# Optimization experiments

Measured on AMD Instinct MI355X. Metric: run time of the kernel, lower is better.

## Reference

```python
import jax, jax.numpy as jnp
import numpy as np

NUM_HEADS = 16
HEAD_DIM = 64
WINDOW = 128        # local attention radius |i-j| <= WINDOW
GLOBAL_STRIDE = 64  # tokens at multiples of GLOBAL_STRIDE attend/are attended globally
NEG_INF = -1e9


def sparse_mask(seq_len):
    # bool [S, S]: local band plus global rows/cols (Longformer-style pattern)
    i = jnp.arange(seq_len)
    local = jnp.abs(i[:, None] - i[None, :]) <= WINDOW
    is_global = (i % GLOBAL_STRIDE) == 0
    return local | is_global[:, None] | is_global[None, :]


def setup_inputs() -> dict:
    key = jax.random.key(0)
    k1, k2, k3 = jax.random.split(key, 3)
    B, S, H = 1, 2048, 1024
    x = jax.random.normal(k1, (B, S, H), dtype=jnp.float32)
    Wqkv = jax.random.normal(k2, (3 * H, H), dtype=jnp.float32) * (1.0 / np.sqrt(H))
    Wout = jax.random.normal(k3, (H, H), dtype=jnp.float32) * (1.0 / np.sqrt(H))
    return {"x": x, "Wqkv": Wqkv, "Wout": Wout}


def reference(x, Wqkv, Wout):
    B, S, H = x.shape
    hd = HEAD_DIM
    scale = 1.0 / np.sqrt(hd)

    qkv = x @ Wqkv.T                       # [B, S, 3H] (torch Linear: x @ W^T)
    q, k, v = jnp.split(qkv, 3, axis=-1)
    # [B, nH, S, hd]
    q = q.reshape(B, S, NUM_HEADS, hd).transpose(0, 2, 1, 3)
    k = k.reshape(B, S, NUM_HEADS, hd).transpose(0, 2, 1, 3)
    v = v.reshape(B, S, NUM_HEADS, hd).transpose(0, 2, 1, 3)

    mask = sparse_mask(S)                  # [S, S] bool, broadcasts over (B, nH)
    scores = jnp.einsum('bhqd,bhkd->bhqk', q, k) * scale
    scores = jnp.where(mask, scores, NEG_INF)
    attn = jax.nn.softmax(scores, axis=-1)  # every row has valid keys -> no NaN
    out = jnp.einsum('bhqk,bhkd->bhqd', attn, v)
    out = out.transpose(0, 2, 1, 3).reshape(B, S, H)
    return out @ Wout.T
```

## Files before the change

kernel.cpp:

```cpp
#include <hip/hip_runtime.h>
#include <hip/hip_bf16.h>
#include <math.h>

#define SEQ   2048
#define HID   1024
#define NH    16
#define HD    64
#define WIN   128
#define GSTR  64
#define NSPL  8

typedef __attribute__((ext_vector_type(8))) short short8;
typedef __attribute__((ext_vector_type(4))) float f32x4;
typedef unsigned short ushort_t;

__device__ inline unsigned short bf16b(float f) {
    union { float f; unsigned int u; } v; v.f = f;
    return (unsigned short)((v.u + 0x7FFFu + ((v.u >> 16) & 1u)) >> 16);
}

#define GLOAD_LDS16(gp, lp)                                                    \
    __builtin_amdgcn_global_load_lds(                                          \
        (const __attribute__((address_space(1))) unsigned int*)(gp),           \
        (__attribute__((address_space(3))) unsigned int*)(lp), 16, 0, 0)

__global__ __launch_bounds__(256) void cvt_bf16(const float4* __restrict__ x,
                                                const float4* __restrict__ wq,
                                                const float4* __restrict__ wo,
                                                ushort4* __restrict__ x16,
                                                ushort4* __restrict__ wq16,
                                                ushort4* __restrict__ wo16) {
    for (int idx = blockIdx.x * 256 + threadIdx.x; idx < 1572864;
         idx += gridDim.x * 256) {
        const float4* src; ushort4* dst; int off;
        if (idx < 524288)       { src = x;  dst = x16;  off = idx; }
        else if (idx < 1310720) { src = wq; dst = wq16; off = idx - 524288; }
        else                    { src = wo; dst = wo16; off = idx - 1310720; }
        float4 v = src[off];
        ushort4 o;
        o.x = bf16b(v.x); o.y = bf16b(v.y); o.z = bf16b(v.z); o.w = bf16b(v.w);
        dst[off] = o;
    }
}

template <int BM, int BN, typename OT>
__global__ __launch_bounds__(256) void gemm_bt16(const unsigned short* __restrict__ A,
                                                 const unsigned short* __restrict__ B,
                                                 OT* __restrict__ C,
                                                 int M, int N, int K) {
    constexpr int MI = BM / 32;
    constexpr int NJ = BN / 32;
    __shared__ unsigned short As[2][BM * 32];
    __shared__ unsigned short Bs[2][BN * 32];

    const int tid  = threadIdx.x;
    const int wave = tid >> 6;
    const int lane = tid & 63;
    const int quad = lane >> 4;
    const int l15  = lane & 15;
    const int bm = blockIdx.y * BM;
    const int bn = blockIdx.x * BN;
    const int wm = (wave & 1) * (BM / 2);
    const int wn = (wave >> 1) * (BN / 2);
    const int srow = lane >> 2;
    const int scol = (lane & 3) * 8;

    f32x4 acc[MI][NJ];
    #pragma unroll
    for (int i = 0; i < MI; ++i)
        #pragma unroll
        for (int j = 0; j < NJ; ++j)
            acc[i][j] = (f32x4){0.f, 0.f, 0.f, 0.f};

    for (int k0 = 0; k0 < K; k0 += 64) {
        #pragma unroll
        for (int hh = 0; hh < 2; ++hh) {
            #pragma unroll
            for (int t = 0; t < BM / 64; ++t) {
                const int row = wave * (BM / 4) + t * 16 + srow;
                GLOAD_LDS16(A + (size_t)(bm + row) * K + k0 + hh * 32 + scol,
                            &As[hh][(size_t)row * 32 + scol]);
            }
            #pragma unroll
            for (int t = 0; t < BN / 64; ++t) {
                const int row = wave * (BN / 4) + t * 16 + srow;
                GLOAD_LDS16(B + (size_t)(bn + row) * K + k0 + hh * 32 + scol,
                            &Bs[hh][(size_t)row * 32 + scol]);
            }
        }
        __syncthreads();

        #pragma unroll
        for (int hh = 0; hh < 2; ++hh) {
            short8 a[MI], b[NJ];
            #pragma unroll
            for (int im = 0; im < MI; ++im)
                a[im] = *(const short8*)&As[hh][(wm + im * 16 + l15) * 32 + quad * 8];
            #pragma unroll
            for (int jn = 0; jn < NJ; ++jn)
                b[jn] = *(const short8*)&Bs[hh][(wn + jn * 16 + l15) * 32 + quad * 8];

            #pragma unroll
            for (int im = 0; im < MI; ++im)
                #pragma unroll
                for (int jn = 0; jn < NJ; ++jn)
                    acc[im][jn] = __builtin_amdgcn_mfma_f32_16x16x32_bf16(
                        b[jn], a[im], acc[im][jn], 0, 0, 0);
        }
        __syncthreads();
    }

    #pragma unroll
    for (int im = 0; im < MI; ++im)
        #pragma unroll
        for (int jn = 0; jn < NJ; ++jn) {
            const int r = bm + wm + im * 16 + l15;
            const int c = bn + wn + jn * 16 + quad * 4;
            if constexpr (sizeof(OT) == 2) {
                ushort4 o;
                o.x = bf16b(acc[im][jn][0]);
                o.y = bf16b(acc[im][jn][1]);
                o.z = bf16b(acc[im][jn][2]);
                o.w = bf16b(acc[im][jn][3]);
                *(ushort4*)&C[(size_t)r * N + c] = o;
            } else {
                *(f32x4*)&C[(size_t)r * N + c] = acc[im][jn];
            }
        }
}

__global__ __launch_bounds__(256) void attn_fused(const unsigned short* __restrict__ qkv16,
                                                  unsigned short* __restrict__ aout16,
                                                  float* __restrict__ pO,
                                                  float* __restrict__ pM,
                                                  float* __restrict__ pL) {
    __shared__ __align__(16) unsigned char smem[38912];
    const int tid = threadIdx.x;
    const int h = blockIdx.y;
    const int w    = tid >> 6;
    const int lane = tid & 63;
    const int quad = lane >> 4;
    const int l15  = lane & 15;

    if (blockIdx.x < 32) {
        ushort_t* Qs = (ushort_t*)smem;
        ushort_t* Ks = (ushort_t*)(smem + 9216);
        ushort_t* Vt = (ushort_t*)(smem + 18432);
        ushort_t* Ps = (ushort_t*)(smem + 27648);

        const int bq = blockIdx.x;
        const int q0 = bq * 64;
        const int qi = q0 + w * 16 + l15;

        for (int f = tid; f < 512; f += 256) {
            int row = f >> 3, c8 = f & 7;
            *(uint4*)&Qs[row * 72 + c8 * 8] =
                *(const uint4*)&qkv16[(size_t)(q0 + row) * (3 * HID) + h * HD + c8 * 8];
        }

        float mq = -1.0e30f, lq = 0.f;
        f32x4 Oacc[4];
        #pragma unroll
        for (int jt = 0; jt < 4; ++jt) Oacc[jt] = (f32x4){0.f, 0.f, 0.f, 0.f};

        const int t0 = max(bq - 2, 0);
        const int t1 = min(bq + 2, SEQ / 64 - 1);

        uint4 pk[2];
        uint2 pva[2], pvb[2];

        auto prefetch = [&](int tt2, bool g2) {
            const int nf = g2 ? 256 : 512;
            #pragma unroll
            for (int u = 0; u < 2; ++u) {
                const int f = tid + u * 256;
                if (f < nf) {
                    const int row = f >> 3, c8 = f & 7;
                    const size_t gb = (size_t)(g2 ? (row << 6) : (tt2 * 64 + row))
                                          * (3 * HID) + HID + h * HD + c8 * 8;
                    pk[u] = *(const uint4*)&qkv16[gb];
                    const int kp = f >> 4, dc = f & 15;
                    const int k0i = 2 * kp, k1i = 2 * kp + 1;
                    const size_t b0 = (size_t)(g2 ? (k0i << 6) : (tt2 * 64 + k0i))
                                          * (3 * HID) + 2 * HID + h * HD + dc * 4;
                    const size_t b1 = (size_t)(g2 ? (k1i << 6) : (tt2 * 64 + k1i))
                                          * (3 * HID) + 2 * HID + h * HD + dc * 4;
                    pva[u] = *(const uint2*)&qkv16[b0];
                    pvb[u] = *(const uint2*)&qkv16[b1];
                }
            }
        };
        auto commit = [&](bool g2) {
            const int nf = g2 ? 256 : 512;
            #pragma unroll
            for (int u = 0; u < 2; ++u) {
                const int f = tid + u * 256;
                if (f < nf) {
                    const int row = f >> 3, c8 = f & 7;
                    *(uint4*)&Ks[row * 72 + c8 * 8] = pk[u];
                    const int kp = f >> 4, dc = f & 15;
                    uint2 va = pva[u], vb = pvb[u];
                    unsigned int w0 = (va.x & 0xFFFFu) | (vb.x << 16);
                    unsigned int w1 = (va.x >> 16)     | (vb.x & 0xFFFF0000u);
                    unsigned int w2 = (va.y & 0xFFFFu) | (vb.y << 16);
                    unsigned int w3 = (va.y >> 16)     | (vb.y & 0xFFFF0000u);
                    *(unsigned int*)&Vt[(dc * 4 + 0) * 72 + 2 * kp] = w0;
                    *(unsigned int*)&Vt[(dc * 4 + 1) * 72 + 2 * kp] = w1;
                    *(unsigned int*)&Vt[(dc * 4 + 2) * 72 + 2 * kp] = w2;
                    *(unsigned int*)&Vt[(dc * 4 + 3) * 72 + 2 * kp] = w3;
                }
            }
        };

        prefetch(t0, false);
        commit(false);
        __syncthreads();

        for (int tt = t0; tt <= t1 + 1; ++tt) {
            const bool gather = (tt == t1 + 1);
            const bool hasnext = (tt < t1 + 1);
            if (hasnext) prefetch(tt + 1, (tt + 1) == t1 + 1);

            short8 bQ0 = *(const short8*)&Qs[(w * 16 + l15) * 72 + quad * 8];
            short8 bQ1 = *(const short8*)&Qs[(w * 16 + l15) * 72 + 32 + quad * 8];
            f32x4 st[4];
            #pragma unroll
            for (int kt = 0; kt < 4; ++kt) {
                short8 aK0 = *(const short8*)&Ks[(kt * 16 + l15) * 72 + quad * 8];
                short8 aK1 = *(const short8*)&Ks[(kt * 16 + l15) * 72 + 32 + quad * 8];
                f32x4 z = (f32x4){0.f, 0.f, 0.f, 0.f};
                z = __builtin_amdgcn_mfma_f32_16x16x32_bf16(aK0, bQ0, z, 0, 0, 0);
                z = __builtin_amdgcn_mfma_f32_16x16x32_bf16(aK1, bQ1, z, 0, 0, 0);
                st[kt] = z;
            }

            float sv[4][4];
            float tm = -1.0e30f;
            #pragma unroll
            for (int kt = 0; kt < 4; ++kt)
                #pragma unroll
                for (int reg = 0; reg < 4; ++reg) {
                    const int c = kt * 16 + quad * 4 + reg;
                    const int j = gather ? (c << 6) : (tt * 64 + c);
                    const bool valid = gather ? ((c < 32) && (abs(qi - j) > WIN))
                                              : (abs(qi - j) <= WIN);
                    sv[kt][reg] = valid ? st[kt][reg] * 0.125f : -1.0e30f;
                    tm = fmaxf(tm, sv[kt][reg]);
                }

            tm = fmaxf(tm, __shfl_xor(tm, 16));
            tm = fmaxf(tm, __shfl_xor(tm, 32));
            const float mn = fmaxf(mq, tm);
            const float alpha = __expf(mq - mn);
            float p[4][4];
            float ts = 0.f;
            #pragma unroll
            for (int kt = 0; kt < 4; ++kt)
                #pragma unroll
                for (int reg = 0; reg < 4; ++reg) {
                    p[kt][reg] = __expf(sv[kt][reg] - mn);
                    ts += p[kt][reg];
                }
            ts += __shfl_xor(ts, 16);
            ts += __shfl_xor(ts, 32);
            lq = lq * alpha + ts;
            mq = mn;

            #pragma unroll
            for (int kt = 0; kt < 4; ++kt) {
                ushort4 pkt;
                pkt.x = bf16b(p[kt][0]); pkt.y = bf16b(p[kt][1]);
                pkt.z = bf16b(p[kt][2]); pkt.w = bf16b(p[kt][3]);
                *(ushort4*)&Ps[(w * 16 + l15) * 72 + kt * 16 + quad * 4] = pkt;
            }
            #pragma unroll
            for (int jt = 0; jt < 4; ++jt) {
                Oacc[jt][0] *= alpha; Oacc[jt][1] *= alpha;
                Oacc[jt][2] *= alpha; Oacc[jt][3] *= alpha;
            }

            short8 bP0 = *(const short8*)&Ps[(w * 16 + l15) * 72 + quad * 8];
            short8 bP1 = *(const short8*)&Ps[(w * 16 + l15) * 72 + 32 + quad * 8];
            #pragma unroll
            for (int jt = 0; jt < 4; ++jt) {
                short8 aV0 = *(const short8*)&Vt[(jt * 16 + l15) * 72 + quad * 8];
                short8 aV1 = *(const short8*)&Vt[(jt * 16 + l15) * 72 + 32 + quad * 8];
                Oacc[jt] = __builtin_amdgcn_mfma_f32_16x16x32_bf16(aV0, bP0, Oacc[jt], 0, 0, 0);
                Oacc[jt] = __builtin_amdgcn_mfma_f32_16x16x32_bf16(aV1, bP1, Oacc[jt], 0, 0, 0);
            }

            if (hasnext) {
                __syncthreads();
                commit((tt + 1) == t1 + 1);
                __syncthreads();
            }
        }

        if (!(w == 0 && l15 == 0)) {
            const float inv = 1.0f / lq;
            #pragma unroll
            for (int jt = 0; jt < 4; ++jt) {
                ushort4 o;
                o.x = bf16b(Oacc[jt][0] * inv);
                o.y = bf16b(Oacc[jt][1] * inv);
                o.z = bf16b(Oacc[jt][2] * inv);
                o.w = bf16b(Oacc[jt][3] * inv);
                *(ushort4*)&aout16[(size_t)qi * HID + h * HD + jt * 16 + quad * 4] = o;
            }
        }
    } else {
        const int sid = blockIdx.x - 32;
        const int gh  = sid / NSPL;
        const int sp  = sid % NSPL;
        ushort_t* Ksw = (ushort_t*)(smem + w * 9728);
        ushort_t* Vtw = (ushort_t*)(smem + w * 9728 + 4608);
        ushort_t* Psw = (ushort_t*)(smem + w * 9728 + 8704);

        const size_t qrow = (size_t)((gh * 16 + l15) * 64) * (3 * HID) + h * HD;
        short8 bQ0 = *(const short8*)&qkv16[qrow + quad * 8];
        short8 bQ1 = *(const short8*)&qkv16[qrow + 32 + quad * 8];

        float mq = -1.0e30f, lq = 0.f;
        f32x4 Oacc[4];
        #pragma unroll
        for (int jt = 0; jt < 4; ++jt) Oacc[jt] = (f32x4){0.f, 0.f, 0.f, 0.f};

        #pragma unroll
        for (int s = 0; s < 2; ++s) {
            const int kb = sp * 256 + w * 64 + s * 32;
            #pragma unroll
            for (int u = 0; u < 4; ++u) {
                const int unit = lane + u * 64;
                const int row = unit >> 3, c8 = unit & 7;
                *(uint4*)&Ksw[row * 72 + c8 * 8] =
                    *(const uint4*)&qkv16[(size_t)(kb + row) * (3 * HID) + HID + h * HD + c8 * 8];
            }
            #pragma unroll
            for (int u = 0; u < 4; ++u) {
                const int unit = lane + u * 64;
                const int kp = unit >> 4, dc = unit & 15;
                const size_t b0 = (size_t)(kb + 2 * kp) * (3 * HID) + 2 * HID + h * HD + dc * 4;
                uint2 va = *(const uint2*)&qkv16[b0];
                uint2 vb = *(const uint2*)&qkv16[b0 + 3 * HID];
                unsigned int w0 = (va.x & 0xFFFFu) | (vb.x << 16);
                unsigned int w1 = (va.x >> 16)     | (vb.x & 0xFFFF0000u);
                unsigned int w2 = (va.y & 0xFFFFu) | (vb.y << 16);
                unsigned int w3 = (va.y >> 16)     | (vb.y & 0xFFFF0000u);
                *(unsigned int*)&Vtw[(dc * 4 + 0) * 32 + 2 * kp] = w0;
                *(unsigned int*)&Vtw[(dc * 4 + 1) * 32 + 2 * kp] = w1;
                *(unsigned int*)&Vtw[(dc * 4 + 2) * 32 + 2 * kp] = w2;
                *(unsigned int*)&Vtw[(dc * 4 + 3) * 32 + 2 * kp] = w3;
            }

            f32x4 st[2];
            #pragma unroll
            for (int kt = 0; kt < 2; ++kt) {
                short8 aK0 = *(const short8*)&Ksw[(kt * 16 + l15) * 72 + quad * 8];
                short8 aK1 = *(const short8*)&Ksw[(kt * 16 + l15) * 72 + 32 + quad * 8];
                f32x4 z = (f32x4){0.f, 0.f, 0.f, 0.f};
                z = __builtin_amdgcn_mfma_f32_16x16x32_bf16(aK0, bQ0, z, 0, 0, 0);
                z = __builtin_amdgcn_mfma_f32_16x16x32_bf16(aK1, bQ1, z, 0, 0, 0);
                st[kt] = z;
            }

            float sv[2][4];
            float tm = -1.0e30f;
            #pragma unroll
            for (int kt = 0; kt < 2; ++kt)
                #pragma unroll
                for (int reg = 0; reg < 4; ++reg) {
                    sv[kt][reg] = st[kt][reg] * 0.125f;
                    tm = fmaxf(tm, sv[kt][reg]);
                }
            tm = fmaxf(tm, __shfl_xor(tm, 16));
            tm = fmaxf(tm, __shfl_xor(tm, 32));
            const float mn = fmaxf(mq, tm);
            const float alpha = __expf(mq - mn);
            float p[2][4];
            float ts = 0.f;
            #pragma unroll
            for (int kt = 0; kt < 2; ++kt)
                #pragma unroll
                for (int reg = 0; reg < 4; ++reg) {
                    p[kt][reg] = __expf(sv[kt][reg] - mn);
                    ts += p[kt][reg];
                }
            ts += __shfl_xor(ts, 16);
            ts += __shfl_xor(ts, 32);
            lq = lq * alpha + ts;
            mq = mn;

            #pragma unroll
            for (int kt = 0; kt < 2; ++kt) {
                ushort4 pkt;
                pkt.x = bf16b(p[kt][0]); pkt.y = bf16b(p[kt][1]);
                pkt.z = bf16b(p[kt][2]); pkt.w = bf16b(p[kt][3]);
                *(ushort4*)&Psw[l15 * 32 + kt * 16 + quad * 4] = pkt;
            }
            #pragma unroll
            for (int jt = 0; jt < 4; ++jt) {
                Oacc[jt][0] *= alpha; Oacc[jt][1] *= alpha;
                Oacc[jt][2] *= alpha; Oacc[jt][3] *= alpha;
            }

            short8 bP = *(const short8*)&Psw[l15 * 32 + quad * 8];
            #pragma unroll
            for (int jt = 0; jt < 4; ++jt) {
                short8 aV = *(const short8*)&Vtw[(jt * 16 + l15) * 32 + quad * 8];
                Oacc[jt] = __builtin_amdgcn_mfma_f32_16x16x32_bf16(aV, bP, Oacc[jt], 0, 0, 0);
            }
        }

        __syncthreads();
        float* Om = (float*)smem;
        float* Ml = (float*)(smem + 16384);
        float* Ll = (float*)(smem + 16640);
        #pragma unroll
        for (int jt = 0; jt < 4; ++jt)
            #pragma unroll
            for (int reg = 0; reg < 4; ++reg)
                Om[(w * 16 + l15) * 64 + jt * 16 + quad * 4 + reg] = Oacc[jt][reg];
        if (quad == 0) { Ml[w * 16 + l15] = mq; Ll[w * 16 + l15] = lq; }
        __syncthreads();

        const int pt = (h * 2 + gh) * NSPL + sp;
        const int d = tid & 63;
        #pragma unroll
        for (int k = 0; k < 4; ++k) {
            const int q = (tid >> 6) * 4 + k;
            float m0 = Ml[q], m1 = Ml[16 + q], m2 = Ml[32 + q], m3 = Ml[48 + q];
            float mM = fmaxf(fmaxf(m0, m1), fmaxf(m2, m3));
            float e0 = __expf(m0 - mM), e1 = __expf(m1 - mM);
            float e2 = __expf(m2 - mM), e3 = __expf(m3 - mM);
            float l = e0 * Ll[q] + e1 * Ll[16 + q] + e2 * Ll[32 + q] + e3 * Ll[48 + q];
            float o = e0 * Om[(q) * 64 + d]        + e1 * Om[(16 + q) * 64 + d]
                    + e2 * Om[(32 + q) * 64 + d]   + e3 * Om[(48 + q) * 64 + d];
            pO[(size_t)pt * 1024 + q * 64 + d] = o;
            if (d == 0) { pM[pt * 16 + q] = mM; pL[pt * 16 + q] = l; }
        }
    }
}

__global__ __launch_bounds__(256) void attn_combine(const float* __restrict__ pO,
                                                    const float* __restrict__ pM,
                                                    const float* __restrict__ pL,
                                                    unsigned short* __restrict__ aout16) {
    const int bid = blockIdx.x;
    const int h = bid >> 1, gh = bid & 1;
    const int base = (h * 2 + gh) * NSPL;
    #pragma unroll
    for (int k = 0; k < 4; ++k) {
        const int idx = threadIdx.x + k * 256;
        const int q = idx >> 6, d = idx & 63;
        float mM = -1.0e30f;
        #pragma unroll
        for (int sp = 0; sp < NSPL; ++sp)
            mM = fmaxf(mM, pM[(base + sp) * 16 + q]);
        float l = 0.f, o = 0.f;
        #pragma unroll
        for (int sp = 0; sp < NSPL; ++sp) {
            const float e = __expf(pM[(base + sp) * 16 + q] - mM);
            l += e * pL[(base + sp) * 16 + q];
            o += e * pO[(size_t)(base + sp) * 1024 + q * 64 + d];
        }
        const int row = (gh * 16 + q) * 64;
        aout16[(size_t)row * HID + h * HD + d] = bf16b(o / l);
    }
}

extern "C" void kernel_launch(void* const* d_in, const int* in_sizes, int n_in,
                              void* d_out, int out_size, void* d_ws, size_t ws_size,
                              hipStream_t stream) {
    const float* x    = (const float*)d_in[0];
    const float* Wqkv = (const float*)d_in[1];
    const float* Wout = (const float*)d_in[2];
    float* out = (float*)d_out;

    unsigned short* x16    = (unsigned short*)d_ws;
    unsigned short* wq16   = x16  + (size_t)SEQ * HID;
    unsigned short* wo16   = wq16 + (size_t)3 * HID * HID;
    unsigned short* qkv16  = wo16 + (size_t)HID * HID;
    unsigned short* aout16 = qkv16 + (size_t)SEQ * 3 * HID;
    float* pO = (float*)(aout16 + (size_t)SEQ * HID);
    float* pM = pO + (size_t)NH * 2 * NSPL * 1024;
    float* pL = pM + (size_t)NH * 2 * NSPL * 16;

    cvt_bf16<<<dim3(1024), 256, 0, stream>>>(
        (const float4*)x, (const float4*)Wqkv, (const float4*)Wout,
        (ushort4*)x16, (ushort4*)wq16, (ushort4*)wo16);

    gemm_bt16<64, 128, unsigned short><<<dim3(3 * HID / 128, SEQ / 64), 256, 0, stream>>>(
        x16, wq16, qkv16, SEQ, 3 * HID, HID);

    attn_fused<<<dim3(32 + 2 * NSPL, NH), 256, 0, stream>>>(
        qkv16, aout16, pO, pM, pL);
    attn_combine<<<dim3(32), 256, 0, stream>>>(pO, pM, pL, aout16);

    gemm_bt16<64, 64, float><<<dim3(HID / 64, SEQ / 64), 256, 0, stream>>>(
        aout16, wo16, out, SEQ, HID, HID);
}
```

Before: 141.6 us.

## Double-buffer GEMM LDS tiles to overlap global loads with MFMA compute

Adds a second LDS buffer to the bf16 GEMM kernel and restructures the K loop so the next K-tile is issued via global_load_lds while the MFMAs consume the current tile. This removes one barrier per iteration and hides global load latency behind compute. The cost is doubled LDS use per block, which may reduce occupancy, and it relies on a single barrier per step being enough to order the asynchronous LDS writes.

```diff
diff --git a/kernel.cpp b/kernel.cpp
--- a/kernel.cpp
+++ b/kernel.cpp
@@ -50,8 +50,8 @@
                                                  int M, int N, int K) {
     constexpr int MI = BM / 32;
     constexpr int NJ = BN / 32;
-    __shared__ unsigned short As[2][BM * 32];
-    __shared__ unsigned short Bs[2][BN * 32];
+    __shared__ unsigned short As[2][2][BM * 32];
+    __shared__ unsigned short Bs[2][2][BN * 32];
 
     const int tid  = threadIdx.x;
     const int wave = tid >> 6;
@@ -72,33 +72,34 @@
         for (int j = 0; j < NJ; ++j)
             acc[i][j] = (f32x4){0.f, 0.f, 0.f, 0.f};
 
-    for (int k0 = 0; k0 < K; k0 += 64) {
+    auto STAGE = [&](int buf, int t) {
+        const int k0 = t * 64;
         #pragma unroll
         for (int hh = 0; hh < 2; ++hh) {
             #pragma unroll
-            for (int t = 0; t < BM / 64; ++t) {
-                const int row = wave * (BM / 4) + t * 16 + srow;
+            for (int tt = 0; tt < BM / 64; ++tt) {
+                const int row = wave * (BM / 4) + tt * 16 + srow;
                 GLOAD_LDS16(A + (size_t)(bm + row) * K + k0 + hh * 32 + scol,
-                            &As[hh][(size_t)row * 32 + scol]);
-            }
-            #pragma unroll
-            for (int t = 0; t < BN / 64; ++t) {
-                const int row = wave * (BN / 4) + t * 16 + srow;
+                            &As[buf][hh][(size_t)row * 32 + scol]);
+            }
+            #pragma unroll
+            for (int tt = 0; tt < BN / 64; ++tt) {
+                const int row = wave * (BN / 4) + tt * 16 + srow;
                 GLOAD_LDS16(B + (size_t)(bn + row) * K + k0 + hh * 32 + scol,
-                            &Bs[hh][(size_t)row * 32 + scol]);
-            }
-        }
-        __syncthreads();
-
+                            &Bs[buf][hh][(size_t)row * 32 + scol]);
+            }
+        }
+    };
+    auto COMPUTE = [&](int buf) {
         #pragma unroll
         for (int hh = 0; hh < 2; ++hh) {
             short8 a[MI], b[NJ];
             #pragma unroll
             for (int im = 0; im < MI; ++im)
-                a[im] = *(const short8*)&As[hh][(wm + im * 16 + l15) * 32 + quad * 8];
+                a[im] = *(const short8*)&As[buf][hh][(wm + im * 16 + l15) * 32 + quad * 8];
             #pragma unroll
             for (int jn = 0; jn < NJ; ++jn)
-                b[jn] = *(const short8*)&Bs[hh][(wn + jn * 16 + l15) * 32 + quad * 8];
+                b[jn] = *(const short8*)&Bs[buf][hh][(wn + jn * 16 + l15) * 32 + quad * 8];
 
             #pragma unroll
             for (int im = 0; im < MI; ++im)
@@ -107,7 +108,27 @@
                     acc[im][jn] = __builtin_amdgcn_mfma_f32_16x16x32_bf16(
                         b[jn], a[im], acc[im][jn], 0, 0, 0);
         }
+    };
+
+    const int NT = K >> 6;
+    STAGE(0, 0);
+    __syncthreads();
+    int t = 0;
+    for (; t + 2 <= NT - 1; t += 2) {
+        STAGE(1, t + 1);
+        COMPUTE(0);
         __syncthreads();
+        STAGE(0, t + 2);
+        COMPUTE(1);
+        __syncthreads();
+    }
+    if (t < NT - 1) {
+        STAGE(1, t + 1);
+        COMPUTE(0);
+        __syncthreads();
+        COMPUTE(1);
+    } else {
+        COMPUTE(0);
     }
 
     #pragma unroll
```

Result: no change. 140.4 us (-0.9%).
